# Performance work log

Hardware: AMD Instinct MI355X
Metric: run time of the kernel (lower is better)

The kernel has to match this reference:

```python
import jax, jax.numpy as jnp
import numpy as np

B = 1024          # batch of positions
K = 64            # king squares
F = 640           # 64 squares * 10 piece types
C = 256           # accumulator channels


def setup_inputs() -> dict:
    key = jax.random.key(0)
    k1, k2, k3 = jax.random.split(key, 3)
    piece_positions = jax.random.randint(k1, (B, 64, 10), 0, 2).astype(jnp.bool_)
    king_positions = jax.random.randint(k2, (B, 2), 0, K, dtype=jnp.int32)
    input_weights = jax.random.normal(k3, (K, F + 1, C), dtype=jnp.float32)
    bias = jnp.zeros((C,), dtype=jnp.float32)
    return {
        "piece_positions": piece_positions,
        "king_positions": king_positions,
        "input_weights": input_weights,
        "bias": bias,
    }


def reference(piece_positions, king_positions, input_weights, bias):
    # Flatten the (64, 10) boolean piece plane into 640 HalfKP features.
    b = piece_positions.shape[0]
    p = piece_positions.reshape(b, F).astype(input_weights.dtype)          # (B, 640)
    # Gather each sample's white/black king weight slabs: (B, 2, 641, 256)
    Wg = jnp.take(input_weights, king_positions, axis=0)
    # Sparse-feature sum for both halves, contracted over feature dim and
    # summed over the two king perspectives in one einsum.
    halves = jnp.einsum("bf,bsfc->bc", p, Wg[:, :, :F, :])                 # (B, 256)
    extra = Wg[:, :, F, :].sum(axis=1)                                     # row 640 for each king
    return halves + extra + bias
```

## Files before the change

### kernel.cpp

```cpp
#include <hip/hip_runtime.h>
#include <hip/hip_bf16.h>


#define F_DIM 640
#define C_DIM 256
#define SLAB_STRIDE (641 * 256)
#define NKING 64
#define LCAP 256

#define WS_CNT_OFF 0
#define WS_LIST_OFF 1024
#define WS_MASK_OFF 66560
#define WS_PART_OFF 148480
#define WS_NEED (WS_PART_OFF + 2 * 1024 * 256 * 4)

typedef float  f32x4  __attribute__((ext_vector_type(4)));
typedef short  bf16x8 __attribute__((ext_vector_type(8)));

__device__ __forceinline__ unsigned f2bf_pk(float a, float b) {
    union { float f; unsigned u; } x, y;
    x.f = a; y.f = b;
    const unsigned ra = (x.u + 0x7FFFu + ((x.u >> 16) & 1u)) >> 16;
    const unsigned rb = (y.u + 0x7FFFu + ((y.u >> 16) & 1u)) >> 16;
    return (ra & 0xFFFFu) | (rb << 16);
}

__device__ __forceinline__ bf16x8 mk_a8(unsigned m32, int g) {
    const unsigned by = (m32 >> (g * 8)) & 0xFFu;
    union { unsigned u[4]; bf16x8 v; } r;
    #pragma unroll
    for (int i = 0; i < 4; ++i)
        r.u[i] = (((by >> (2 * i)) & 1u) ? 0x3F80u : 0u) |
                 (((by >> (2 * i + 1)) & 1u) ? 0x3F800000u : 0u);
    return r.v;
}

__global__ __launch_bounds__(256)
void pack_and_lists(const int* __restrict__ pieces, const int* __restrict__ kings,
                    unsigned long long* __restrict__ mask,
                    int* __restrict__ cnt, int* __restrict__ list,
                    int nwords, int nent)
{
    const int gtid = blockIdx.x * 256 + threadIdx.x;
    const int gw = blockIdx.x * 4 + (threadIdx.x >> 6);
    const int lane = threadIdx.x & 63;
    if (gw < nwords) {
        const int v = pieces[(size_t)gw * 64 + lane];
        const unsigned long long m = __ballot(v != 0);
        if (lane == 0) mask[gw] = m;
    }
    if (gtid < nent) {
        const int b = gtid >> 1, p = gtid & 1;
        const int kk = kings[2 * b + p];
        const int pos = atomicAdd(&cnt[kk], 1);
        if (pos < LCAP) list[kk * LCAP + pos] = gtid;
    }
}

__global__ __launch_bounds__(512, 4)
void halfkp_mfma(const float* __restrict__ W,
                 const unsigned long long* __restrict__ mask,
                 const int* __restrict__ cnt,
                 const int* __restrict__ list,
                 float* __restrict__ partial)
{
    const int k  = blockIdx.x;
    const int cq = blockIdx.y;
    const int t  = threadIdx.x;
    const int wv = t >> 6, lane = t & 63;
    const int g = lane >> 4, li = lane & 15;
    const int c0 = cq * 32 + li;

    __shared__ int s_ent[64];
    __shared__ unsigned s_m32[64][21];
    __shared__ f32x4 s_red[4][8][64];

    const int n_k = min(cnt[k], LCAP);
    const float* __restrict__ Wk = W + (size_t)k * SLAB_STRIDE;

    for (int mb = 0; mb < n_k; mb += 64) {
        const int nc = min(n_k - mb, 64);

        if (t < 64) s_ent[t] = (t < nc) ? list[k * LCAP + mb + t] : -1;
        __syncthreads();

        for (int idx = t; idx < 64 * 21; idx += 512) {
            const int row = idx & 63, ks = idx >> 6;
            const int id = s_ent[row];
            unsigned v = 0;
            if (id >= 0) {
                if (ks < 20) {
                    const unsigned long long mw = mask[(size_t)(id >> 1) * 10 + (ks >> 1)];
                    v = (unsigned)(mw >> ((ks & 1) * 32));
                } else {
                    v = 1u;
                }
            }
            s_m32[row][ks] = v;
        }
        __syncthreads();

        f32x4 acc[4][2];
        #pragma unroll
        for (int mt = 0; mt < 4; ++mt) {
            acc[mt][0] = (f32x4){0.f, 0.f, 0.f, 0.f};
            acc[mt][1] = (f32x4){0.f, 0.f, 0.f, 0.f};
        }

        #pragma unroll
        for (int i = 0; i < 3; ++i) {
            const int ks = wv + 8 * i;
            if (ks < 21) {
                bf16x8 bf[2];
                #pragma unroll
                for (int nt = 0; nt < 2; ++nt) {
                    float wt[8];
                    #pragma unroll
                    for (int j = 0; j < 8; ++j) {
                        const int f = min(ks * 32 + g * 8 + j, F_DIM);
                        wt[j] = Wk[(size_t)f * C_DIM + c0 + nt * 16];
                    }
                    union { unsigned u[4]; bf16x8 v; } bb;
                    #pragma unroll
                    for (int j = 0; j < 4; ++j)
                        bb.u[j] = f2bf_pk(wt[2 * j], wt[2 * j + 1]);
                    bf[nt] = bb.v;
                }
                #pragma unroll
                for (int mt = 0; mt < 4; ++mt) {
                    const bf16x8 af = mk_a8(s_m32[mt * 16 + li][ks], g);
                    acc[mt][0] = __builtin_amdgcn_mfma_f32_16x16x32_bf16(af, bf[0], acc[mt][0], 0, 0, 0);
                    acc[mt][1] = __builtin_amdgcn_mfma_f32_16x16x32_bf16(af, bf[1], acc[mt][1], 0, 0, 0);
                }
            }
        }

        __syncthreads();
        if (wv >= 4) {
            #pragma unroll
            for (int mt = 0; mt < 4; ++mt) {
                s_red[wv - 4][mt * 2 + 0][lane] = acc[mt][0];
                s_red[wv - 4][mt * 2 + 1][lane] = acc[mt][1];
            }
        }
        __syncthreads();
        if (wv < 4) {
            #pragma unroll
            for (int mt = 0; mt < 4; ++mt) {
                acc[mt][0] += s_red[wv][mt * 2 + 0][lane];
                acc[mt][1] += s_red[wv][mt * 2 + 1][lane];
            }
        }
        __syncthreads();
        if (wv == 2 || wv == 3) {
            #pragma unroll
            for (int mt = 0; mt < 4; ++mt) {
                s_red[wv - 2][mt * 2 + 0][lane] = acc[mt][0];
                s_red[wv - 2][mt * 2 + 1][lane] = acc[mt][1];
            }
        }
        __syncthreads();
        if (wv < 2) {
            #pragma unroll
            for (int mt = 0; mt < 4; ++mt) {
                acc[mt][0] += s_red[wv][mt * 2 + 0][lane];
                acc[mt][1] += s_red[wv][mt * 2 + 1][lane];
            }
        }
        __syncthreads();
        if (wv == 1) {
            #pragma unroll
            for (int mt = 0; mt < 4; ++mt) {
                s_red[0][mt * 2 + 0][lane] = acc[mt][0];
                s_red[0][mt * 2 + 1][lane] = acc[mt][1];
            }
        }
        __syncthreads();
        if (wv == 0) {
            #pragma unroll
            for (int mt = 0; mt < 4; ++mt) {
                acc[mt][0] += s_red[0][mt * 2 + 0][lane];
                acc[mt][1] += s_red[0][mt * 2 + 1][lane];
            }
            #pragma unroll
            for (int mt = 0; mt < 4; ++mt) {
                #pragma unroll
                for (int i = 0; i < 4; ++i) {
                    const int row = mt * 16 + 4 * g + i;
                    if (row < nc) {
                        const int id = s_ent[row];
                        const size_t o = (((size_t)(id & 1)) * 1024 + (id >> 1)) * C_DIM;
                        partial[o + c0]      = acc[mt][0][i];
                        partial[o + c0 + 16] = acc[mt][1][i];
                    }
                }
            }
        }
        __syncthreads();
    }
}

__global__ __launch_bounds__(256)
void finalize(const float* __restrict__ partial,
              const float* __restrict__ bias,
              float* __restrict__ out)
{
    const int i = blockIdx.x * 256 + threadIdx.x;
    const float4 b4 = ((const float4*)bias)[i & 63];
    const float4 p0 = ((const float4*)partial)[i];
    const float4 p1 = ((const float4*)partial)[1024 * 64 + i];
    float4 o;
    o.x = b4.x + p0.x + p1.x;
    o.y = b4.y + p0.y + p1.y;
    o.z = b4.z + p0.z + p1.z;
    o.w = b4.w + p0.w + p1.w;
    ((float4*)out)[i] = o;
}

__global__ __launch_bounds__(256)
void halfkp_fallback(const int* __restrict__ pieces, const int* __restrict__ kings,
                     const float* __restrict__ W, const float* __restrict__ bias,
                     float* __restrict__ out)
{
    const int b = blockIdx.x;
    const int c = threadIdx.x;
    const int lane = c & 63;
    const int k0 = kings[2 * b + 0];
    const int k1 = kings[2 * b + 1];
    const float* W0 = W + (size_t)k0 * SLAB_STRIDE + c;
    const float* W1 = W + (size_t)k1 * SLAB_STRIDE + c;
    float acc = bias[c] + W0[640 * 256] + W1[640 * 256];
    const int* pi = pieces + (size_t)b * F_DIM;
    #pragma unroll
    for (int ch = 0; ch < 10; ++ch) {
        int v = pi[ch * 64 + lane];
        unsigned long long m = __ballot(v != 0);
        const float* b0 = W0 + ch * 64 * 256;
        const float* b1 = W1 + ch * 64 * 256;
        while (m) {
            const int f = __builtin_ctzll(m);
            m &= m - 1;
            acc += b0[f * 256] + b1[f * 256];
        }
    }
    out[(size_t)b * C_DIM + c] = acc;
}

extern "C" void kernel_launch(void* const* d_in, const int* in_sizes, int n_in,
                              void* d_out, int out_size, void* d_ws, size_t ws_size,
                              hipStream_t stream) {
    const int* pieces = (const int*)d_in[0];
    const int* kings  = (const int*)d_in[1];
    const float* W    = (const float*)d_in[2];
    const float* bias = (const float*)d_in[3];
    float* out        = (float*)d_out;

    const int B = in_sizes[1] / 2;
    const int nent = 2 * B;
    const int nwords = B * 10;

    if (ws_size < (size_t)WS_NEED) {
        halfkp_fallback<<<dim3(B), dim3(C_DIM), 0, stream>>>(pieces, kings, W, bias, out);
        return;
    }

    int* cnt  = (int*)((char*)d_ws + WS_CNT_OFF);
    int* list = (int*)((char*)d_ws + WS_LIST_OFF);
    unsigned long long* mask = (unsigned long long*)((char*)d_ws + WS_MASK_OFF);
    float* part = (float*)((char*)d_ws + WS_PART_OFF);

    hipMemsetAsync(cnt, 0, NKING * sizeof(int), stream);
    pack_and_lists<<<dim3((nwords + 3) / 4), dim3(256), 0, stream>>>(pieces, kings, mask, cnt, list, nwords, nent);
    halfkp_mfma<<<dim3(NKING, 8), dim3(512), 0, stream>>>(W, mask, cnt, list, part);
    finalize<<<dim3(B * 64 / 256), dim3(256), 0, stream>>>(part, bias, out);
}
```

Before: 28.79 us.

## Build per-king lists in-block via ballot and split waves by output tile

```diff
diff --git a/kernel.cpp b/kernel.cpp
--- a/kernel.cpp
+++ b/kernel.cpp
@@ -7,11 +7,10 @@
 #define SLAB_STRIDE (641 * 256)
 #define NKING 64
 #define LCAP 256
-
-#define WS_CNT_OFF 0
-#define WS_LIST_OFF 1024
-#define WS_MASK_OFF 66560
-#define WS_PART_OFF 148480
+#define NC_MAX 64
+
+#define WS_MASK_OFF 0
+#define WS_PART_OFF 81920
 #define WS_NEED (WS_PART_OFF + 2 * 1024 * 256 * 4)
 
 typedef float  f32x4  __attribute__((ext_vector_type(4)));
@@ -36,57 +35,81 @@
 }
 
 __global__ __launch_bounds__(256)
-void pack_and_lists(const int* __restrict__ pieces, const int* __restrict__ kings,
-                    unsigned long long* __restrict__ mask,
-                    int* __restrict__ cnt, int* __restrict__ list,
-                    int nwords, int nent)
-{
-    const int gtid = blockIdx.x * 256 + threadIdx.x;
+void pack_masks(const int* __restrict__ pieces,
+                unsigned long long* __restrict__ mask,
+                int nwords)
+{
     const int gw = blockIdx.x * 4 + (threadIdx.x >> 6);
     const int lane = threadIdx.x & 63;
-    if (gw < nwords) {
-        const int v = pieces[(size_t)gw * 64 + lane];
-        const unsigned long long m = __ballot(v != 0);
-        if (lane == 0) mask[gw] = m;
-    }
-    if (gtid < nent) {
-        const int b = gtid >> 1, p = gtid & 1;
-        const int kk = kings[2 * b + p];
-        const int pos = atomicAdd(&cnt[kk], 1);
-        if (pos < LCAP) list[kk * LCAP + pos] = gtid;
-    }
+    if (gw >= nwords) return;
+    const int v = pieces[(size_t)gw * 64 + lane];
+    const unsigned long long m = __ballot(v != 0);
+    if (lane == 0) mask[gw] = m;
 }
 
 __global__ __launch_bounds__(512, 4)
 void halfkp_mfma(const float* __restrict__ W,
                  const unsigned long long* __restrict__ mask,
-                 const int* __restrict__ cnt,
-                 const int* __restrict__ list,
-                 float* __restrict__ partial)
+                 const int* __restrict__ kings,
+                 float* __restrict__ partial,
+                 int nent)
 {
     const int k  = blockIdx.x;
     const int cq = blockIdx.y;
     const int t  = threadIdx.x;
     const int wv = t >> 6, lane = t & 63;
-    const int g = lane >> 4, li = lane & 15;
-    const int c0 = cq * 32 + li;
-
-    __shared__ int s_ent[64];
+    const int mt = wv & 3, ntc = wv >> 2;
+    const int li = lane & 15, g = lane >> 4;
+    const int col = cq * 32 + ntc * 16 + li;
+
+    __shared__ int s_ent[LCAP];
+    __shared__ int s_cb[NC_MAX + 1];
     __shared__ unsigned s_m32[64][21];
-    __shared__ f32x4 s_red[4][8][64];
-
-    const int n_k = min(cnt[k], LCAP);
+    __shared__ int s_nk;
+
+    const int NC = nent >> 6;
+    const int nit = NC >> 3;
+    unsigned long long mm[8];
+    #pragma unroll
+    for (int it = 0; it < 8; ++it) {
+        if (it < nit) {
+            const int c = wv + (it << 3);
+            const int kk = kings[(c << 6) + lane];
+            mm[it] = __ballot(kk == k);
+            if (lane == 0) s_cb[c] = (int)__popcll(mm[it]);
+        }
+    }
+    __syncthreads();
+    if (t == 0) {
+        int s = 0;
+        for (int c = 0; c < NC; ++c) { const int v = s_cb[c]; s_cb[c] = s; s += v; }
+        s_cb[NC] = s;
+        s_nk = min(s, LCAP);
+    }
+    __syncthreads();
+    const unsigned long long lt = (1ull << lane) - 1ull;
+    #pragma unroll
+    for (int it = 0; it < 8; ++it) {
+        if (it < nit) {
+            const int c = wv + (it << 3);
+            if ((mm[it] >> lane) & 1ull) {
+                const int pos = s_cb[c] + (int)__popcll(mm[it] & lt);
+                if (pos < LCAP) s_ent[pos] = (c << 6) + lane;
+            }
+        }
+    }
+    __syncthreads();
+    const int n_k = s_nk;
+
     const float* __restrict__ Wk = W + (size_t)k * SLAB_STRIDE;
+    const float* __restrict__ Wc = Wk + col;
 
     for (int mb = 0; mb < n_k; mb += 64) {
         const int nc = min(n_k - mb, 64);
 
-        if (t < 64) s_ent[t] = (t < nc) ? list[k * LCAP + mb + t] : -1;
-        __syncthreads();
-
         for (int idx = t; idx < 64 * 21; idx += 512) {
             const int row = idx & 63, ks = idx >> 6;
-            const int id = s_ent[row];
+            const int id = (row < nc) ? s_ent[mb + row] : -1;
             unsigned v = 0;
             if (id >= 0) {
                 if (ks < 20) {
@@ -100,100 +123,29 @@
         }
         __syncthreads();
 
-        f32x4 acc[4][2];
+        f32x4 acc = {0.f, 0.f, 0.f, 0.f};
+        #pragma unroll 3
+        for (int ks = 0; ks < 21; ++ks) {
+            float wt[8];
+            #pragma unroll
+            for (int j = 0; j < 8; ++j) {
+                const int f = min(ks * 32 + g * 8 + j, F_DIM);
+                wt[j] = Wc[(size_t)f * C_DIM];
+            }
+            union { unsigned u[4]; bf16x8 v; } bb;
+            #pragma unroll
+            for (int j = 0; j < 4; ++j)
+                bb.u[j] = f2bf_pk(wt[2 * j], wt[2 * j + 1]);
+            const bf16x8 af = mk_a8(s_m32[mt * 16 + li][ks], g);
+            acc = __builtin_amdgcn_mfma_f32_16x16x32_bf16(af, bb.v, acc, 0, 0, 0);
+        }
+
         #pragma unroll
-        for (int mt = 0; mt < 4; ++mt) {
-            acc[mt][0] = (f32x4){0.f, 0.f, 0.f, 0.f};
-            acc[mt][1] = (f32x4){0.f, 0.f, 0.f, 0.f};
-        }
-
-        #pragma unroll
-        for (int i = 0; i < 3; ++i) {
-            const int ks = wv + 8 * i;
-            if (ks < 21) {
-                bf16x8 bf[2];
-                #pragma unroll
-                for (int nt = 0; nt < 2; ++nt) {
-                    float wt[8];
-                    #pragma unroll
-                    for (int j = 0; j < 8; ++j) {
-                        const int f = min(ks * 32 + g * 8 + j, F_DIM);
-                        wt[j] = Wk[(size_t)f * C_DIM + c0 + nt * 16];
-                    }
-                    union { unsigned u[4]; bf16x8 v; } bb;
-                    #pragma unroll
-                    for (int j = 0; j < 4; ++j)
-                        bb.u[j] = f2bf_pk(wt[2 * j], wt[2 * j + 1]);
-                    bf[nt] = bb.v;
-                }
-                #pragma unroll
-                for (int mt = 0; mt < 4; ++mt) {
-                    const bf16x8 af = mk_a8(s_m32[mt * 16 + li][ks], g);
-                    acc[mt][0] = __builtin_amdgcn_mfma_f32_16x16x32_bf16(af, bf[0], acc[mt][0], 0, 0, 0);
-                    acc[mt][1] = __builtin_amdgcn_mfma_f32_16x16x32_bf16(af, bf[1], acc[mt][1], 0, 0, 0);
-                }
-            }
-        }
-
-        __syncthreads();
-        if (wv >= 4) {
-            #pragma unroll
-            for (int mt = 0; mt < 4; ++mt) {
-                s_red[wv - 4][mt * 2 + 0][lane] = acc[mt][0];
-                s_red[wv - 4][mt * 2 + 1][lane] = acc[mt][1];
-            }
-        }
-        __syncthreads();
-        if (wv < 4) {
-            #pragma unroll
-            for (int mt = 0; mt < 4; ++mt) {
-                acc[mt][0] += s_red[wv][mt * 2 + 0][lane];
-                acc[mt][1] += s_red[wv][mt * 2 + 1][lane];
-            }
-        }
-        __syncthreads();
-        if (wv == 2 || wv == 3) {
-            #pragma unroll
-            for (int mt = 0; mt < 4; ++mt) {
-                s_red[wv - 2][mt * 2 + 0][lane] = acc[mt][0];
-                s_red[wv - 2][mt * 2 + 1][lane] = acc[mt][1];
-            }
-        }
-        __syncthreads();
-        if (wv < 2) {
-            #pragma unroll
-            for (int mt = 0; mt < 4; ++mt) {
-                acc[mt][0] += s_red[wv][mt * 2 + 0][lane];
-                acc[mt][1] += s_red[wv][mt * 2 + 1][lane];
-            }
-        }
-        __syncthreads();
-        if (wv == 1) {
-            #pragma unroll
-            for (int mt = 0; mt < 4; ++mt) {
-                s_red[0][mt * 2 + 0][lane] = acc[mt][0];
-                s_red[0][mt * 2 + 1][lane] = acc[mt][1];
-            }
-        }
-        __syncthreads();
-        if (wv == 0) {
-            #pragma unroll
-            for (int mt = 0; mt < 4; ++mt) {
-                acc[mt][0] += s_red[0][mt * 2 + 0][lane];
-                acc[mt][1] += s_red[0][mt * 2 + 1][lane];
-            }
-            #pragma unroll
-            for (int mt = 0; mt < 4; ++mt) {
-                #pragma unroll
-                for (int i = 0; i < 4; ++i) {
-                    const int row = mt * 16 + 4 * g + i;
-                    if (row < nc) {
-                        const int id = s_ent[row];
-                        const size_t o = (((size_t)(id & 1)) * 1024 + (id >> 1)) * C_DIM;
-                        partial[o + c0]      = acc[mt][0][i];
-                        partial[o + c0 + 16] = acc[mt][1][i];
-                    }
-                }
+        for (int i = 0; i < 4; ++i) {
+            const int row = mt * 16 + 4 * g + i;
+            if (row < nc) {
+                const int id = s_ent[mb + row];
+                partial[(((size_t)(id & 1)) * 1024 + (id >> 1)) * C_DIM + col] = acc[i];
             }
         }
         __syncthreads();
@@ -264,13 +216,10 @@
         return;
     }
 
-    int* cnt  = (int*)((char*)d_ws + WS_CNT_OFF);
-    int* list = (int*)((char*)d_ws + WS_LIST_OFF);
     unsigned long long* mask = (unsigned long long*)((char*)d_ws + WS_MASK_OFF);
     float* part = (float*)((char*)d_ws + WS_PART_OFF);
 
-    hipMemsetAsync(cnt, 0, NKING * sizeof(int), stream);
-    pack_and_lists<<<dim3((nwords + 3) / 4), dim3(256), 0, stream>>>(pieces, kings, mask, cnt, list, nwords, nent);
-    halfkp_mfma<<<dim3(NKING, 8), dim3(512), 0, stream>>>(W, mask, cnt, list, part);
+    pack_masks<<<dim3((nwords + 3) / 4), dim3(256), 0, stream>>>(pieces, mask, nwords);
+    halfkp_mfma<<<dim3(NKING, 8), dim3(512), 0, stream>>>(W, mask, kings, part, nent);
     finalize<<<dim3(B * 64 / 256), dim3(256), 0, stream>>>(part, bias, out);
 }
```

New measurement: 27.43 us. -4.7%, faster.
